# Kernel optimization log

Measured on AMD Instinct MI355X. Metric: run time of the kernel, lower is better.

The kernel has to match this reference:

```python
import jax, jax.numpy as jnp
import numpy as np

B, N, M, DQ, DK, DV, H = 8, 1024, 1024, 512, 512, 512, 8
DS = DV // H  # dim_split = 64
NEG = -1e38


def _ln(x, g, b, eps=1e-5):
    mu = jnp.mean(x, -1, keepdims=True)
    var = jnp.mean((x - mu) ** 2, -1, keepdims=True)
    return (x - mu) * jax.lax.rsqrt(var + eps) * g + b


def setup_inputs() -> dict:
    key = jax.random.key(0)
    ks = jax.random.split(key, 16)
    s = 0.02
    return {
        "x": jax.random.normal(ks[0], (B, N, DQ), jnp.float32),
        "y": jax.random.normal(ks[1], (B, M, DK), jnp.float32),
        "x_mask": jax.random.randint(ks[2], (B, N), 0, 2).astype(bool),
        "y_mask": jax.random.randint(ks[3], (B, M), 0, 2).astype(bool),
        "Wq": jax.random.normal(ks[4], (DQ, DV), jnp.float32) * s,
        "Wk": jax.random.normal(ks[5], (DK, DV), jnp.float32) * s,
        "Wv": jax.random.normal(ks[6], (DK, DV), jnp.float32) * s,
        "Wo": jax.random.normal(ks[7], (DV, DQ), jnp.float32) * s,
        "W1": jax.random.normal(ks[8], (DQ, DQ), jnp.float32) * s,
        "b1": jnp.zeros((DQ,), jnp.float32),
        "W2": jax.random.normal(ks[9], (DQ, DQ), jnp.float32) * s,
        "b2": jnp.zeros((DQ,), jnp.float32),
        "g1": jnp.ones((DQ,), jnp.float32),
        "be1": jnp.zeros((DQ,), jnp.float32),
        "g2": jnp.ones((DQ,), jnp.float32),
        "be2": jnp.zeros((DQ,), jnp.float32),
    }


def reference(x, y, x_mask, y_mask, Wq, Wk, Wv, Wo, W1, b1, W2, b2, g1, be1, g2, be2):
    xm = x_mask[..., None]  # [B,N,1]
    ym = y_mask[..., None]  # [B,M,1]
    x = jnp.where(xm, 0.0, x)
    y = jnp.where(ym, 0.0, y)
    # projections (no bias); masked rows stay zero, re-mask as in source
    q = jnp.where(xm, 0.0, x @ Wq).reshape(B, N, H, DS)
    k = jnp.where(ym, 0.0, y @ Wk).reshape(B, M, H, DS)
    v = jnp.where(ym, 0.0, y @ Wv).reshape(B, M, H, DS)
    # scaled dot product; NOTE: scale is sqrt(dim_v), faithful to source
    sdp = jnp.einsum('bnhd,bmhd->bhnm', q, k) / np.sqrt(DV)
    mask = x_mask[:, None, :, None] | y_mask[:, None, None, :]  # [B,1,N,M]
    sdp = jnp.where(mask, NEG, sdp)
    alpha = jax.nn.softmax(sdp, axis=-1)  # softmax over keys (slot_att=False)
    att = jnp.einsum('bhnm,bmhd->bnhd', alpha, v).reshape(B, N, DV)
    att = jnp.where(xm, 0.0, att)
    o = x + att @ Wo
    o = _ln(o, g1, be1)
    ff = jax.nn.relu(o @ W1 + b1) @ W2 + b2
    o = _ln(o + ff, g2, be2)
    return jnp.where(xm, 0.0, o)
```

## Files before the change

kernel.cpp:

```cpp
#include <hip/hip_runtime.h>
#include <hip/hip_bf16.h>

typedef __bf16 bf16;
typedef __attribute__((ext_vector_type(4))) __bf16 bf16x4;
typedef __attribute__((ext_vector_type(8))) __bf16 bf16x8;
typedef __attribute__((ext_vector_type(4))) float f32x4;

#define B_ 8
#define N_ 1024
#define M_ 1024
#define H_ 8
#define ROWS_ (B_ * N_)

__device__ __forceinline__ f32x4 mfma16(bf16x8 a, bf16x8 b, f32x4 c) {
    return __builtin_amdgcn_mfma_f32_16x16x32_bf16(a, b, c, 0, 0, 0);
}

__device__ __forceinline__ void glds16(const void* g, void* l) {
    __builtin_amdgcn_global_load_lds((const __attribute__((address_space(1))) void*)g,
                                     (__attribute__((address_space(3))) void*)l, 16, 0, 0);
}

__global__ __launch_bounds__(256) void prep(const float* __restrict__ x, const float* __restrict__ y,
                                            bf16* __restrict__ Xb, bf16* __restrict__ Yb,
                                            const float* W0, const float* W1, const float* W2,
                                            const float* W3, const float* W4, const float* W5,
                                            bf16* T0, bf16* T1, bf16* T2, bf16* T3, bf16* T4, bf16* T5) {
    __shared__ float t[64][65];
    int bid = blockIdx.x;
    if (bid < 8192) {
        int i = bid * 256 + threadIdx.x;
        const float4* s;
        bf16x4* d;
        int j;
        if (i < 1048576) { s = (const float4*)x; d = (bf16x4*)Xb; j = i; }
        else             { s = (const float4*)y; d = (bf16x4*)Yb; j = i - 1048576; }
        float4 f = s[j];
        bf16x4 o = {(bf16)f.x, (bf16)f.y, (bf16)f.z, (bf16)f.w};
        d[j] = o;
        return;
    }
    int wb = bid - 8192;
    const float* srcs[6] = {W0, W1, W2, W3, W4, W5};
    bf16* dsts[6] = {T0, T1, T2, T3, T4, T5};
    const float* W = srcs[wb >> 6];
    bf16* Wt = dsts[wb >> 6];
    int tile = wb & 63;
    int k0 = (tile >> 3) * 64, n0 = (tile & 7) * 64;
    int tx = threadIdx.x & 63, ty = threadIdx.x >> 6;
#pragma unroll
    for (int j = 0; j < 16; ++j)
        t[ty + j * 4][tx] = W[(size_t)(k0 + ty + j * 4) * 512 + n0 + tx];
    __syncthreads();
#pragma unroll
    for (int j = 0; j < 16; ++j)
        Wt[(size_t)(n0 + ty + j * 4) * 512 + k0 + tx] = (bf16)t[tx][ty + j * 4];
}

__device__ __forceinline__ void gemm_core(const bf16* __restrict__ A, const bf16* __restrict__ Bt,
                                          int row0, int col0, char* AsB, char* BsB, f32x4 acc[2][4]) {
    int tid = threadIdx.x, wave = tid >> 6, lane = tid & 63;
    int lr = lane & 15, q4 = lane >> 4;
    const bf16 *Asrc[4], *Bsrc[2];
#pragma unroll
    for (int s = 0; s < 4; ++s) {
        int c = tid + s * 256, r = c >> 3, bk = (c & 7) ^ (r & 7);
        Asrc[s] = A + (size_t)(row0 + r) * 512 + bk * 8;
    }
#pragma unroll
    for (int s = 0; s < 2; ++s) {
        int c = tid + s * 256, r = c >> 3, bk = (c & 7) ^ (r & 7);
        Bsrc[s] = Bt + (size_t)(col0 + r) * 512 + bk * 8;
    }
    int wb = wave * 1024;
#pragma unroll
    for (int s = 0; s < 4; ++s) glds16(Asrc[s], AsB + s * 4096 + wb);
#pragma unroll
    for (int s = 0; s < 2; ++s) glds16(Bsrc[s], BsB + s * 4096 + wb);
#pragma unroll
    for (int it = 0; it < 8; ++it) {
        __syncthreads();
        const char* Ac = AsB + (it & 1) * 16384;
        const char* Bc = BsB + (it & 1) * 8192;
        if (it < 7) {
            char* An = AsB + ((it + 1) & 1) * 16384;
            char* Bn = BsB + ((it + 1) & 1) * 8192;
            int k0 = (it + 1) * 64;
#pragma unroll
            for (int s = 0; s < 4; ++s) glds16(Asrc[s] + k0, An + s * 4096 + wb);
#pragma unroll
            for (int s = 0; s < 2; ++s) glds16(Bsrc[s] + k0, Bn + s * 4096 + wb);
        }
        bf16x8 af[2][2], bfr[4][2];
#pragma unroll
        for (int rt = 0; rt < 2; ++rt) {
            int row = wave * 32 + rt * 16 + lr;
#pragma unroll
            for (int c = 0; c < 2; ++c)
                af[rt][c] = *(const bf16x8*)(Ac + (row * 8 + ((c * 4 + q4) ^ (row & 7))) * 16);
        }
#pragma unroll
        for (int ct = 0; ct < 4; ++ct) {
            int col = ct * 16 + lr;
#pragma unroll
            for (int c = 0; c < 2; ++c)
                bfr[ct][c] = *(const bf16x8*)(Bc + (col * 8 + ((c * 4 + q4) ^ (col & 7))) * 16);
        }
#pragma unroll
        for (int rt = 0; rt < 2; ++rt)
#pragma unroll
            for (int ct = 0; ct < 4; ++ct) {
                acc[rt][ct] = mfma16(af[rt][0], bfr[ct][0], acc[rt][ct]);
                acc[rt][ct] = mfma16(af[rt][1], bfr[ct][1], acc[rt][ct]);
            }
    }
}

__global__ __launch_bounds__(256, 2) void proj_qkv(const bf16* __restrict__ Xb, const bf16* __restrict__ Yb,
                                                   const bf16* __restrict__ Wqt, const bf16* __restrict__ Wkt,
                                                   const bf16* __restrict__ Wvt,
                                                   bf16* __restrict__ qb, bf16* __restrict__ kb,
                                                   bf16* __restrict__ Vt) {
    __shared__ char AsB[2 * 16384];
    __shared__ char BsB[2 * 8192];
    int z = blockIdx.z;
    const bf16 *A, *Bt;
    int row0, col0;
    if (z == 0)      { A = Xb;  Bt = Wqt; row0 = blockIdx.x * 128; col0 = blockIdx.y * 64; }
    else if (z == 1) { A = Yb;  Bt = Wkt; row0 = blockIdx.x * 128; col0 = blockIdx.y * 64; }
    else { A = Wvt; Bt = Yb; int flat = blockIdx.y * 64 + blockIdx.x; row0 = (flat & 3) * 128; col0 = (flat >> 2) * 64; }
    const f32x4 z4 = {0.f, 0.f, 0.f, 0.f};
    f32x4 acc[2][4] = {{z4, z4, z4, z4}, {z4, z4, z4, z4}};
    gemm_core(A, Bt, row0, col0, AsB, BsB, acc);
    int wave = threadIdx.x >> 6, lane = threadIdx.x & 63, lr = lane & 15, q4 = lane >> 4;
    bf16* dst = (z == 0) ? qb : kb;
#pragma unroll
    for (int rt = 0; rt < 2; ++rt)
#pragma unroll
        for (int ct = 0; ct < 4; ++ct) {
            int col = col0 + ct * 16 + lr;
#pragma unroll
            for (int r = 0; r < 4; ++r) {
                int row = row0 + wave * 32 + rt * 16 + q4 * 4 + r;
                bf16 v = (bf16)acc[rt][ct][r];
                if (z < 2) dst[(size_t)row * 512 + col] = v;
                else Vt[(size_t)((col >> 10) * 512 + row) * 1024 + (col & 1023)] = v;
            }
        }
}

template <int MODE>
__global__ __launch_bounds__(256, 2) void gemm_bt(const bf16* __restrict__ A, const bf16* __restrict__ Bt,
                                                  const float* __restrict__ bias, void* __restrict__ Cout) {
    __shared__ char AsB[2 * 16384];
    __shared__ char BsB[2 * 8192];
    int row0 = blockIdx.x * 128, col0 = blockIdx.y * 64;
    const f32x4 z4 = {0.f, 0.f, 0.f, 0.f};
    f32x4 acc[2][4] = {{z4, z4, z4, z4}, {z4, z4, z4, z4}};
    gemm_core(A, Bt, row0, col0, AsB, BsB, acc);
    int wave = threadIdx.x >> 6, lane = threadIdx.x & 63, lr = lane & 15, q4 = lane >> 4;
#pragma unroll
    for (int rt = 0; rt < 2; ++rt)
#pragma unroll
        for (int ct = 0; ct < 4; ++ct) {
            int col = col0 + ct * 16 + lr;
            float bv = (MODE >= 2) ? bias[col] : 0.0f;
#pragma unroll
            for (int r = 0; r < 4; ++r) {
                int row = row0 + wave * 32 + rt * 16 + q4 * 4 + r;
                float v = acc[rt][ct][r] + bv;
                if (MODE == 3) v = fmaxf(v, 0.0f);
                if (MODE == 3) ((bf16*)Cout)[(size_t)row * 512 + col] = (bf16)v;
                else           ((float*)Cout)[(size_t)row * 512 + col] = v;
            }
        }
}

__global__ __launch_bounds__(256, 4) void attn(const bf16* __restrict__ Q, const bf16* __restrict__ Kb,
                                               const bf16* __restrict__ Vt, const int* __restrict__ ymask,
                                               bf16* __restrict__ att) {
    __shared__ bf16 Ks[64 * 64];
    __shared__ bf16 Vs[64 * 64];
    __shared__ bf16 Ps[4][16 * 72];
    __shared__ float fmk[1024];

    int bid = blockIdx.x;
    int bh = bid & 63, n0 = (bid >> 6) * 64;
    int b = bh >> 3, h = bh & 7;
    int tid = threadIdx.x, wave = tid >> 6, lane = tid & 63;
    int lr = lane & 15, q4 = lane >> 4;
    const float cl = 0.06376373228f;

    const int* ymb = ymask + (b << 10);
#pragma unroll
    for (int j = 0; j < 4; ++j) {
        int i = tid + j * 256;
        fmk[i] = ymb[i] ? -1e38f : 0.0f;
    }

    const bf16* qp = Q + (size_t)((b << 10) + n0 + wave * 16 + lr) * 512 + h * 64 + q4 * 8;
    bf16x8 aq0 = *(const bf16x8*)qp;
    bf16x8 aq1 = *(const bf16x8*)(qp + 32);

    const bf16 *Ksrc[2], *Vsrc[2];
#pragma unroll
    for (int s = 0; s < 2; ++s) {
        int c = tid + s * 256, r = c >> 3, bk = (c & 7) ^ (r & 7);
        Ksrc[s] = Kb + (size_t)((b << 10) + r) * 512 + h * 64 + bk * 8;
        Vsrc[s] = Vt + (size_t)(b * 512 + h * 64 + r) * 1024 + bk * 8;
    }
    int wb = wave * 1024;

    const f32x4 zv = {0.f, 0.f, 0.f, 0.f};
    f32x4 O[4] = {zv, zv, zv, zv};
    float lsum[4] = {0.f, 0.f, 0.f, 0.f};

    for (int it = 0; it < 16; ++it) {
        __syncthreads();
        size_t m0 = (size_t)it * 64;
#pragma unroll
        for (int s = 0; s < 2; ++s) {
            glds16(Ksrc[s] + m0 * 512, (char*)Ks + s * 4096 + wb);
            glds16(Vsrc[s] + m0, (char*)Vs + s * 4096 + wb);
        }
        __syncthreads();

#pragma unroll
        for (int nt = 0; nt < 4; ++nt) {
            int krow = nt * 16 + lr;
            bf16x8 kf0 = *(const bf16x8*)((const char*)Ks + (krow * 8 + (q4 ^ (krow & 7))) * 16);
            bf16x8 kf1 = *(const bf16x8*)((const char*)Ks + (krow * 8 + ((4 + q4) ^ (krow & 7))) * 16);
            float fm = fmk[it * 64 + krow];
            f32x4 s = {fm, fm, fm, fm};
            s = mfma16(aq0, kf0, s);
            s = mfma16(aq1, kf1, s);
#pragma unroll
            for (int rr = 0; rr < 4; ++rr) {
                float p = exp2f(s[rr] * cl);
                lsum[rr] += p;
                Ps[wave][(q4 * 4 + rr) * 72 + krow] = (bf16)p;
            }
        }
        bf16x8 ap0 = *(const bf16x8*)&Ps[wave][lr * 72 + q4 * 8];
        bf16x8 ap1 = *(const bf16x8*)&Ps[wave][lr * 72 + 32 + q4 * 8];
#pragma unroll
        for (int dt = 0; dt < 4; ++dt) {
            int vrow = dt * 16 + lr;
            bf16x8 vf0 = *(const bf16x8*)((const char*)Vs + (vrow * 8 + (q4 ^ (vrow & 7))) * 16);
            bf16x8 vf1 = *(const bf16x8*)((const char*)Vs + (vrow * 8 + ((4 + q4) ^ (vrow & 7))) * 16);
            O[dt] = mfma16(ap0, vf0, O[dt]);
            O[dt] = mfma16(ap1, vf1, O[dt]);
        }
    }

#pragma unroll
    for (int rr = 0; rr < 4; ++rr) {
        float v = lsum[rr];
        v += __shfl_xor(v, 1); v += __shfl_xor(v, 2);
        v += __shfl_xor(v, 4); v += __shfl_xor(v, 8);
        lsum[rr] = (v > 0.0f) ? (1.0f / v) : 0.0f;
    }
#pragma unroll
    for (int dt = 0; dt < 4; ++dt)
#pragma unroll
        for (int rr = 0; rr < 4; ++rr) {
            int row = n0 + wave * 16 + q4 * 4 + rr;
            att[(size_t)((b << 10) + row) * 512 + h * 64 + dt * 16 + lr] =
                (bf16)(O[dt][rr] * lsum[rr]);
        }
}

__global__ __launch_bounds__(128) void ln1_k(const float* __restrict__ X, const float* __restrict__ R,
                                             const float* __restrict__ g, const float* __restrict__ be,
                                             float* __restrict__ O, bf16* __restrict__ Obf) {
    int row = blockIdx.x, t = threadIdx.x;
    float4 xv = ((const float4*)(X + (size_t)row * 512))[t];
    float4 rv = ((const float4*)(R + (size_t)row * 512))[t];
    float4 o = {xv.x + rv.x, xv.y + rv.y, xv.z + rv.z, xv.w + rv.w};
    float s = o.x + o.y + o.z + o.w;
    float sq = o.x * o.x + o.y * o.y + o.z * o.z + o.w * o.w;
#pragma unroll
    for (int off = 1; off < 64; off <<= 1) { s += __shfl_xor(s, off); sq += __shfl_xor(sq, off); }
    __shared__ float ls[2], lq[2];
    if ((t & 63) == 0) { ls[t >> 6] = s; lq[t >> 6] = sq; }
    __syncthreads();
    s = ls[0] + ls[1]; sq = lq[0] + lq[1];
    float mu = s * (1.0f / 512.0f);
    float var = sq * (1.0f / 512.0f) - mu * mu;
    float rs = rsqrtf(var + 1e-5f);
    float4 gv = ((const float4*)g)[t];
    float4 bv = ((const float4*)be)[t];
    float4 r4 = {(o.x - mu) * rs * gv.x + bv.x, (o.y - mu) * rs * gv.y + bv.y,
                 (o.z - mu) * rs * gv.z + bv.z, (o.w - mu) * rs * gv.w + bv.w};
    ((float4*)(O + (size_t)row * 512))[t] = r4;
    bf16x4 b4 = {(bf16)r4.x, (bf16)r4.y, (bf16)r4.z, (bf16)r4.w};
    ((bf16x4*)(Obf + (size_t)row * 512))[t] = b4;
}

__global__ __launch_bounds__(128) void ln2_k(const float* __restrict__ O, const float* __restrict__ F,
                                             const float* __restrict__ g, const float* __restrict__ be,
                                             const int* __restrict__ xmask, float* __restrict__ out) {
    int row = blockIdx.x, t = threadIdx.x;
    float4 xv = ((const float4*)(O + (size_t)row * 512))[t];
    float4 rv = ((const float4*)(F + (size_t)row * 512))[t];
    float4 o = {xv.x + rv.x, xv.y + rv.y, xv.z + rv.z, xv.w + rv.w};
    float s = o.x + o.y + o.z + o.w;
    float sq = o.x * o.x + o.y * o.y + o.z * o.z + o.w * o.w;
#pragma unroll
    for (int off = 1; off < 64; off <<= 1) { s += __shfl_xor(s, off); sq += __shfl_xor(sq, off); }
    __shared__ float ls[2], lq[2];
    if ((t & 63) == 0) { ls[t >> 6] = s; lq[t >> 6] = sq; }
    __syncthreads();
    s = ls[0] + ls[1]; sq = lq[0] + lq[1];
    float mu = s * (1.0f / 512.0f);
    float var = sq * (1.0f / 512.0f) - mu * mu;
    float rs = rsqrtf(var + 1e-5f);
    int msk = xmask[row];
    float4 gv = ((const float4*)g)[t];
    float4 bv = ((const float4*)be)[t];
    float4 r4 = {(o.x - mu) * rs * gv.x + bv.x, (o.y - mu) * rs * gv.y + bv.y,
                 (o.z - mu) * rs * gv.z + bv.z, (o.w - mu) * rs * gv.w + bv.w};
    if (msk) r4 = {0.f, 0.f, 0.f, 0.f};
    ((float4*)(out + (size_t)row * 512))[t] = r4;
}

extern "C" void kernel_launch(void* const* d_in, const int* in_sizes, int n_in,
                              void* d_out, int out_size, void* d_ws, size_t ws_size,
                              hipStream_t stream) {
    const float* x   = (const float*)d_in[0];
    const float* y   = (const float*)d_in[1];
    const int*   xm  = (const int*)d_in[2];
    const int*   ym  = (const int*)d_in[3];
    const float* Wq  = (const float*)d_in[4];
    const float* Wk  = (const float*)d_in[5];
    const float* Wv  = (const float*)d_in[6];
    const float* Wo  = (const float*)d_in[7];
    const float* W1  = (const float*)d_in[8];
    const float* b1  = (const float*)d_in[9];
    const float* W2  = (const float*)d_in[10];
    const float* b2  = (const float*)d_in[11];
    const float* g1  = (const float*)d_in[12];
    const float* be1 = (const float*)d_in[13];
    const float* g2  = (const float*)d_in[14];
    const float* be2 = (const float*)d_in[15];

    char* ws = (char*)d_ws;
    const size_t WT_SZ  = 512 * 512 * sizeof(bf16);
    const size_t XB_SZ  = (size_t)ROWS_ * 512 * sizeof(bf16);
    const size_t F32_SZ = (size_t)ROWS_ * 512 * sizeof(float);

    bf16* Wqt = (bf16*)(ws + 0 * WT_SZ);
    bf16* Wkt = (bf16*)(ws + 1 * WT_SZ);
    bf16* Wvt = (bf16*)(ws + 2 * WT_SZ);
    bf16* Wot = (bf16*)(ws + 3 * WT_SZ);
    bf16* W1t = (bf16*)(ws + 4 * WT_SZ);
    bf16* W2t = (bf16*)(ws + 5 * WT_SZ);
    size_t off = 6 * WT_SZ;
    bf16* Xb  = (bf16*)(ws + off); off += XB_SZ;
    bf16* Yb  = (bf16*)(ws + off); off += XB_SZ;
    bf16* qb  = (bf16*)(ws + off); off += XB_SZ;
    bf16* kb  = (bf16*)(ws + off); off += XB_SZ;
    bf16* Vt  = (bf16*)(ws + off); off += XB_SZ;
    float* awo = (float*)(ws + off); off += F32_SZ;
    float* ob  = (float*)(ws + off); off += F32_SZ;
    bf16* attb = Xb;
    bf16* obf  = qb;
    bf16* hb   = Yb;
    float* fb  = awo;

    prep<<<8576, 256, 0, stream>>>(x, y, Xb, Yb, Wq, Wk, Wv, Wo, W1, W2,
                                   Wqt, Wkt, Wvt, Wot, W1t, W2t);

    proj_qkv<<<dim3(64, 8, 3), 256, 0, stream>>>(Xb, Yb, Wqt, Wkt, Wvt, qb, kb, Vt);

    attn<<<1024, 256, 0, stream>>>(qb, kb, Vt, ym, attb);

    dim3 gg(64, 8);
    gemm_bt<0><<<gg, 256, 0, stream>>>(attb, Wot, nullptr, awo);
    ln1_k<<<ROWS_, 128, 0, stream>>>(x, awo, g1, be1, ob, obf);
    gemm_bt<3><<<gg, 256, 0, stream>>>(obf, W1t, b1, hb);
    gemm_bt<2><<<gg, 256, 0, stream>>>(hb, W2t, b2, fb);
    ln2_k<<<ROWS_, 128, 0, stream>>>(ob, fb, g2, be2, xm, (float*)d_out);
}
```

Baseline: 226.2 us.

## Double-buffer attention K/V tiles and store intermediate activations as bf16

The attention kernel now uses 512-thread blocks covering 128 query rows, with double-buffered K/V shared-memory tiles. The next tile's global-to-LDS load is issued while the current tile is being computed, which removes one barrier per iteration. The Wo, W1 and W2 GEMM outputs and the LN1 output are now written only as bf16, and the fp32 intermediate buffers are dropped. This cuts memory traffic in the GEMM epilogues and layernorm kernels, at the cost of lower precision in the residual path into LN2.

```diff
diff --git a/kernel.cpp b/kernel.cpp
--- a/kernel.cpp
+++ b/kernel.cpp
@@ -149,9 +149,9 @@
         }
 }
 
-template <int MODE>
+template <int BIAS, int RELU>
 __global__ __launch_bounds__(256, 2) void gemm_bt(const bf16* __restrict__ A, const bf16* __restrict__ Bt,
-                                                  const float* __restrict__ bias, void* __restrict__ Cout) {
+                                                  const float* __restrict__ bias, bf16* __restrict__ Cout) {
     __shared__ char AsB[2 * 16384];
     __shared__ char BsB[2 * 8192];
     int row0 = blockIdx.x * 128, col0 = blockIdx.y * 64;
@@ -164,72 +164,67 @@
 #pragma unroll
         for (int ct = 0; ct < 4; ++ct) {
             int col = col0 + ct * 16 + lr;
-            float bv = (MODE >= 2) ? bias[col] : 0.0f;
+            float bv = BIAS ? bias[col] : 0.0f;
 #pragma unroll
             for (int r = 0; r < 4; ++r) {
                 int row = row0 + wave * 32 + rt * 16 + q4 * 4 + r;
                 float v = acc[rt][ct][r] + bv;
-                if (MODE == 3) v = fmaxf(v, 0.0f);
-                if (MODE == 3) ((bf16*)Cout)[(size_t)row * 512 + col] = (bf16)v;
-                else           ((float*)Cout)[(size_t)row * 512 + col] = v;
+                if (RELU) v = fmaxf(v, 0.0f);
+                Cout[(size_t)row * 512 + col] = (bf16)v;
             }
         }
 }
 
-__global__ __launch_bounds__(256, 4) void attn(const bf16* __restrict__ Q, const bf16* __restrict__ Kb,
+__global__ __launch_bounds__(512, 2) void attn(const bf16* __restrict__ Q, const bf16* __restrict__ Kb,
                                                const bf16* __restrict__ Vt, const int* __restrict__ ymask,
                                                bf16* __restrict__ att) {
-    __shared__ bf16 Ks[64 * 64];
-    __shared__ bf16 Vs[64 * 64];
-    __shared__ bf16 Ps[4][16 * 72];
+    __shared__ bf16 Ks[2][64 * 64];
+    __shared__ bf16 Vs[2][64 * 64];
+    __shared__ bf16 Ps[8][16 * 72];
     __shared__ float fmk[1024];
 
     int bid = blockIdx.x;
-    int bh = bid & 63, n0 = (bid >> 6) * 64;
+    int bh = bid & 63, n0 = (bid >> 6) * 128;
     int b = bh >> 3, h = bh & 7;
     int tid = threadIdx.x, wave = tid >> 6, lane = tid & 63;
     int lr = lane & 15, q4 = lane >> 4;
     const float cl = 0.06376373228f;
 
     const int* ymb = ymask + (b << 10);
-#pragma unroll
-    for (int j = 0; j < 4; ++j) {
-        int i = tid + j * 256;
-        fmk[i] = ymb[i] ? -1e38f : 0.0f;
-    }
+    fmk[tid]       = ymb[tid]       ? -1e38f : 0.0f;
+    fmk[tid + 512] = ymb[tid + 512] ? -1e38f : 0.0f;
 
     const bf16* qp = Q + (size_t)((b << 10) + n0 + wave * 16 + lr) * 512 + h * 64 + q4 * 8;
     bf16x8 aq0 = *(const bf16x8*)qp;
     bf16x8 aq1 = *(const bf16x8*)(qp + 32);
 
-    const bf16 *Ksrc[2], *Vsrc[2];
-#pragma unroll
-    for (int s = 0; s < 2; ++s) {
-        int c = tid + s * 256, r = c >> 3, bk = (c & 7) ^ (r & 7);
-        Ksrc[s] = Kb + (size_t)((b << 10) + r) * 512 + h * 64 + bk * 8;
-        Vsrc[s] = Vt + (size_t)(b * 512 + h * 64 + r) * 1024 + bk * 8;
-    }
-    int wb = wave * 1024;
+    int r = tid >> 3, bk = (tid & 7) ^ (r & 7);
+    const bf16* Ksrc = Kb + (size_t)((b << 10) + r) * 512 + h * 64 + bk * 8;
+    const bf16* Vsrc = Vt + (size_t)(b * 512 + h * 64 + r) * 1024 + bk * 8;
+    int ldso = tid * 16;
 
     const f32x4 zv = {0.f, 0.f, 0.f, 0.f};
     f32x4 O[4] = {zv, zv, zv, zv};
     float lsum[4] = {0.f, 0.f, 0.f, 0.f};
 
+    glds16(Ksrc, (char*)Ks[0] + ldso);
+    glds16(Vsrc, (char*)Vs[0] + ldso);
+
     for (int it = 0; it < 16; ++it) {
         __syncthreads();
-        size_t m0 = (size_t)it * 64;
-#pragma unroll
-        for (int s = 0; s < 2; ++s) {
-            glds16(Ksrc[s] + m0 * 512, (char*)Ks + s * 4096 + wb);
-            glds16(Vsrc[s] + m0, (char*)Vs + s * 4096 + wb);
-        }
-        __syncthreads();
+        const char* K_ = (const char*)Ks[it & 1];
+        const char* V_ = (const char*)Vs[it & 1];
+        if (it < 15) {
+            size_t m1 = (size_t)(it + 1) * 64;
+            glds16(Ksrc + m1 * 512, (char*)Ks[(it + 1) & 1] + ldso);
+            glds16(Vsrc + m1, (char*)Vs[(it + 1) & 1] + ldso);
+        }
 
 #pragma unroll
         for (int nt = 0; nt < 4; ++nt) {
             int krow = nt * 16 + lr;
-            bf16x8 kf0 = *(const bf16x8*)((const char*)Ks + (krow * 8 + (q4 ^ (krow & 7))) * 16);
-            bf16x8 kf1 = *(const bf16x8*)((const char*)Ks + (krow * 8 + ((4 + q4) ^ (krow & 7))) * 16);
+            bf16x8 kf0 = *(const bf16x8*)(K_ + (krow * 8 + (q4 ^ (krow & 7))) * 16);
+            bf16x8 kf1 = *(const bf16x8*)(K_ + (krow * 8 + ((4 + q4) ^ (krow & 7))) * 16);
             float fm = fmk[it * 64 + krow];
             f32x4 s = {fm, fm, fm, fm};
             s = mfma16(aq0, kf0, s);
@@ -246,8 +241,8 @@
 #pragma unroll
         for (int dt = 0; dt < 4; ++dt) {
             int vrow = dt * 16 + lr;
-            bf16x8 vf0 = *(const bf16x8*)((const char*)Vs + (vrow * 8 + (q4 ^ (vrow & 7))) * 16);
-            bf16x8 vf1 = *(const bf16x8*)((const char*)Vs + (vrow * 8 + ((4 + q4) ^ (vrow & 7))) * 16);
+            bf16x8 vf0 = *(const bf16x8*)(V_ + (vrow * 8 + (q4 ^ (vrow & 7))) * 16);
+            bf16x8 vf1 = *(const bf16x8*)(V_ + (vrow * 8 + ((4 + q4) ^ (vrow & 7))) * 16);
             O[dt] = mfma16(ap0, vf0, O[dt]);
             O[dt] = mfma16(ap1, vf1, O[dt]);
         }
@@ -270,13 +265,13 @@
         }
 }
 
-__global__ __launch_bounds__(128) void ln1_k(const float* __restrict__ X, const float* __restrict__ R,
+__global__ __launch_bounds__(128) void ln1_k(const float* __restrict__ X, const bf16* __restrict__ A,
                                              const float* __restrict__ g, const float* __restrict__ be,
-                                             float* __restrict__ O, bf16* __restrict__ Obf) {
+                                             bf16* __restrict__ Obf) {
     int row = blockIdx.x, t = threadIdx.x;
     float4 xv = ((const float4*)(X + (size_t)row * 512))[t];
-    float4 rv = ((const float4*)(R + (size_t)row * 512))[t];
-    float4 o = {xv.x + rv.x, xv.y + rv.y, xv.z + rv.z, xv.w + rv.w};
+    bf16x4 av = ((const bf16x4*)(A + (size_t)row * 512))[t];
+    float4 o = {xv.x + (float)av.x, xv.y + (float)av.y, xv.z + (float)av.z, xv.w + (float)av.w};
     float s = o.x + o.y + o.z + o.w;
     float sq = o.x * o.x + o.y * o.y + o.z * o.z + o.w * o.w;
 #pragma unroll
@@ -290,20 +285,19 @@
     float rs = rsqrtf(var + 1e-5f);
     float4 gv = ((const float4*)g)[t];
     float4 bv = ((const float4*)be)[t];
-    float4 r4 = {(o.x - mu) * rs * gv.x + bv.x, (o.y - mu) * rs * gv.y + bv.y,
-                 (o.z - mu) * rs * gv.z + bv.z, (o.w - mu) * rs * gv.w + bv.w};
-    ((float4*)(O + (size_t)row * 512))[t] = r4;
-    bf16x4 b4 = {(bf16)r4.x, (bf16)r4.y, (bf16)r4.z, (bf16)r4.w};
+    bf16x4 b4 = {(bf16)((o.x - mu) * rs * gv.x + bv.x), (bf16)((o.y - mu) * rs * gv.y + bv.y),
+                 (bf16)((o.z - mu) * rs * gv.z + bv.z), (bf16)((o.w - mu) * rs * gv.w + bv.w)};
     ((bf16x4*)(Obf + (size_t)row * 512))[t] = b4;
 }
 
-__global__ __launch_bounds__(128) void ln2_k(const float* __restrict__ O, const float* __restrict__ F,
+__global__ __launch_bounds__(128) void ln2_k(const bf16* __restrict__ Ob, const bf16* __restrict__ F,
                                              const float* __restrict__ g, const float* __restrict__ be,
                                              const int* __restrict__ xmask, float* __restrict__ out) {
     int row = blockIdx.x, t = threadIdx.x;
-    float4 xv = ((const float4*)(O + (size_t)row * 512))[t];
-    float4 rv = ((const float4*)(F + (size_t)row * 512))[t];
-    float4 o = {xv.x + rv.x, xv.y + rv.y, xv.z + rv.z, xv.w + rv.w};
+    bf16x4 xv = ((const bf16x4*)(Ob + (size_t)row * 512))[t];
+    bf16x4 rv = ((const bf16x4*)(F + (size_t)row * 512))[t];
+    float4 o = {(float)xv.x + (float)rv.x, (float)xv.y + (float)rv.y,
+                (float)xv.z + (float)rv.z, (float)xv.w + (float)rv.w};
     float s = o.x + o.y + o.z + o.w;
     float sq = o.x * o.x + o.y * o.y + o.z * o.z + o.w * o.w;
 #pragma unroll
@@ -347,7 +341,6 @@
     char* ws = (char*)d_ws;
     const size_t WT_SZ  = 512 * 512 * sizeof(bf16);
     const size_t XB_SZ  = (size_t)ROWS_ * 512 * sizeof(bf16);
-    const size_t F32_SZ = (size_t)ROWS_ * 512 * sizeof(float);
 
     bf16* Wqt = (bf16*)(ws + 0 * WT_SZ);
     bf16* Wkt = (bf16*)(ws + 1 * WT_SZ);
@@ -361,24 +354,23 @@
     bf16* qb  = (bf16*)(ws + off); off += XB_SZ;
     bf16* kb  = (bf16*)(ws + off); off += XB_SZ;
     bf16* Vt  = (bf16*)(ws + off); off += XB_SZ;
-    float* awo = (float*)(ws + off); off += F32_SZ;
-    float* ob  = (float*)(ws + off); off += F32_SZ;
     bf16* attb = Xb;
+    bf16* awo  = kb;
     bf16* obf  = qb;
     bf16* hb   = Yb;
-    float* fb  = awo;
+    bf16* fb   = Vt;
 
     prep<<<8576, 256, 0, stream>>>(x, y, Xb, Yb, Wq, Wk, Wv, Wo, W1, W2,
                                    Wqt, Wkt, Wvt, Wot, W1t, W2t);
 
     proj_qkv<<<dim3(64, 8, 3), 256, 0, stream>>>(Xb, Yb, Wqt, Wkt, Wvt, qb, kb, Vt);
 
-    attn<<<1024, 256, 0, stream>>>(qb, kb, Vt, ym, attb);
+    attn<<<512, 512, 0, stream>>>(qb, kb, Vt, ym, attb);
 
     dim3 gg(64, 8);
-    gemm_bt<0><<<gg, 256, 0, stream>>>(attb, Wot, nullptr, awo);
-    ln1_k<<<ROWS_, 128, 0, stream>>>(x, awo, g1, be1, ob, obf);
-    gemm_bt<3><<<gg, 256, 0, stream>>>(obf, W1t, b1, hb);
-    gemm_bt<2><<<gg, 256, 0, stream>>>(hb, W2t, b2, fb);
-    ln2_k<<<ROWS_, 128, 0, stream>>>(ob, fb, g2, be2, xm, (float*)d_out);
-}
+    gemm_bt<0, 0><<<gg, 256, 0, stream>>>(attb, Wot, nullptr, awo);
+    ln1_k<<<ROWS_, 128, 0, stream>>>(x, awo, g1, be1, obf);
+    gemm_bt<1, 1><<<gg, 256, 0, stream>>>(obf, W1t, b1, hb);
+    gemm_bt<1, 0><<<gg, 256, 0, stream>>>(hb, W2t, b2, fb);
+    ln2_k<<<ROWS_, 128, 0, stream>>>(obf, fb, g2, be2, xm, (float*)d_out);
+}
```

Result: faster. 220.3 us (-2.6%).
